# Performance work log

Hardware: AMD Instinct MI355X
Metric: run time of the kernel (lower is better)

The kernel has to match this reference:

```python
import jax, jax.numpy as jnp
import numpy as np


def setup_inputs() -> dict:
    key = jax.random.key(0)
    ks = jax.random.split(key, 6)
    B, C, S, E = 8, 16, 512, 256
    wscale = (2.0 / (E + E)) ** 0.5  # xavier_normal for [E, E] fan_in=fan_out=E
    return {
        "query": jax.random.normal(ks[0], (B, C, S, E), dtype=jnp.float32),
        "key": jax.random.normal(ks[1], (B, C, S, E), dtype=jnp.float32),
        "value": jax.random.normal(ks[2], (B, C, S, E), dtype=jnp.float32),
        "q_proj_weight": jax.random.normal(ks[3], (C, E, E), dtype=jnp.float32) * wscale,
        "k_proj_weight": jax.random.normal(ks[4], (C, E, E), dtype=jnp.float32) * wscale,
        "v_proj_weight": jax.random.normal(ks[5], (C, E, E), dtype=jnp.float32) * wscale,
        "q_proj_bias": jnp.zeros((C, 1, E), dtype=jnp.float32),
        "k_proj_bias": jnp.zeros((C, 1, E), dtype=jnp.float32),
        "v_proj_bias": jnp.zeros((C, 1, E), dtype=jnp.float32),
    }


def reference(query, key, value, q_proj_weight, k_proj_weight, v_proj_weight,
              q_proj_bias, k_proj_bias, v_proj_bias):
    E = query.shape[-1]
    # Per-cycle projection + bias + ReLU.  b=batch, c=cycle, s/t=seq, e/f=embed
    q = jax.nn.relu(jnp.einsum("bcse,cef->bcsf", query, q_proj_weight) + q_proj_bias)
    k = jax.nn.relu(jnp.einsum("bcse,cef->bcsf", key, k_proj_weight) + k_proj_bias)
    v = jax.nn.relu(jnp.einsum("bcse,cef->bcsf", value, v_proj_weight) + v_proj_bias)
    q = q * (float(E) ** -0.5)
    attn = jax.nn.softmax(jnp.einsum("bcse,bcte->bcst", q, k), axis=-1)
    out = jnp.einsum("bcst,bcte->bcse", attn, v)
    return out
```

## Files before the change

kernel.cpp:

```cpp
#include <hip/hip_runtime.h>

constexpr int BATCH = 8;
constexpr int CYC   = 16;
constexpr int SEQ   = 512;
constexpr int EMB   = 256;

typedef __attribute__((ext_vector_type(8))) short bf16x8;
typedef __attribute__((ext_vector_type(4))) float f32x4;

__device__ __forceinline__ unsigned short f2bf(float x) {
    unsigned int u = __float_as_uint(x);
    u += 0x7fffu + ((u >> 16) & 1u);
    return (unsigned short)(u >> 16);
}
__device__ __forceinline__ unsigned int pk2(float lo, float hi) {
    return (unsigned int)f2bf(lo) | ((unsigned int)f2bf(hi) << 16);
}
__device__ __forceinline__ f32x4 mfma16(bf16x8 a, bf16x8 b, f32x4 c) {
    return __builtin_amdgcn_mfma_f32_16x16x32_bf16(a, b, c, 0, 0, 0);
}
__device__ __forceinline__ void gll16(const void* g, void* l) {
    __builtin_amdgcn_global_load_lds(
        (const __attribute__((address_space(1))) void*)g,
        (__attribute__((address_space(3))) void*)l, 16, 0, 0);
}
union BCast { int4 i; bf16x8 v; };

__global__ __launch_bounds__(256) void wt_kernel(
    const float* __restrict__ Wq, const float* __restrict__ Wk,
    const float* __restrict__ Wv,
    unsigned short* __restrict__ Tq, unsigned short* __restrict__ Tk,
    unsigned short* __restrict__ Tv)
{
    __shared__ float tile[64][65];
    const int z = blockIdx.z;
    const int which = z >> 4, c = z & 15;
    const float* W = which == 0 ? Wq : which == 1 ? Wk : Wv;
    unsigned short* Wt = which == 0 ? Tq : which == 1 ? Tk : Tv;
    const int e0 = blockIdx.x * 64;
    const int f0 = blockIdx.y * 64;
    const float* Wc = W + (size_t)c * EMB * EMB;
    unsigned short* Wtc = Wt + (size_t)c * EMB * EMB;
    const int t = threadIdx.x;
    {
        const int er = t >> 4;
        const int fc = (t & 15) * 4;
        for (int i = 0; i < 4; ++i) {
            const float4 v = *(const float4*)(Wc + (size_t)(e0 + er + i * 16) * EMB + f0 + fc);
            tile[er + i * 16][fc + 0] = v.x;
            tile[er + i * 16][fc + 1] = v.y;
            tile[er + i * 16][fc + 2] = v.z;
            tile[er + i * 16][fc + 3] = v.w;
        }
    }
    __syncthreads();
    {
        const int fr = t >> 4;
        const int ec = (t & 15) * 4;
        for (int i = 0; i < 4; ++i) {
            const int f = fr + i * 16;
            ushort4 o;
            o.x = f2bf(tile[ec + 0][f]);
            o.y = f2bf(tile[ec + 1][f]);
            o.z = f2bf(tile[ec + 2][f]);
            o.w = f2bf(tile[ec + 3][f]);
            *(ushort4*)(Wtc + (size_t)(f0 + f) * EMB + e0 + ec) = o;
        }
    }
}

__global__ __launch_bounds__(256, 3) void proj_kernel(
    const float* __restrict__ Xq, const float* __restrict__ Xk,
    const float* __restrict__ Xv,
    const unsigned short* __restrict__ Wq, const unsigned short* __restrict__ Wk,
    const unsigned short* __restrict__ Wv,
    const float* __restrict__ Bq, const float* __restrict__ Bk,
    const float* __restrict__ Bv,
    unsigned short* __restrict__ Yq, unsigned short* __restrict__ Yk,
    unsigned short* __restrict__ Yv)
{
    __shared__ float          As[2][64 * 32];
    __shared__ unsigned short Bs[2][256 * 32];

    const int z = blockIdx.z;
    const float* X = z == 0 ? Xq : z == 1 ? Xk : Xv;
    const unsigned short* Wt = z == 0 ? Wq : z == 1 ? Wk : Wv;
    const float* bias = z == 0 ? Bq : z == 1 ? Bk : Bv;
    unsigned short* Y = z == 0 ? Yq : z == 1 ? Yk : Yv;
    const float scale = z == 0 ? 0.0625f : 1.0f;

    const int bc = blockIdx.x;
    const int c  = bc & (CYC - 1);
    const int m0 = blockIdx.y * 64;
    const float* Xb = X + (size_t)bc * SEQ * EMB;
    const unsigned short* Wc = Wt + (size_t)c * EMB * EMB;
    const float* bb = bias + (size_t)c * EMB;
    unsigned short* Yb = Y + (size_t)bc * SEQ * EMB;

    const int tid  = threadIdx.x;
    const int lane = tid & 63, w = tid >> 6;
    const int ln   = lane & 15, quad = lane >> 4;
    const int wu   = __builtin_amdgcn_readfirstlane(w);

    const int arow = lane >> 3;
    const int achk = (lane & 7) ^ arow;
    const int brow = lane >> 2;
    const int gch  = (lane & 3) ^ ((lane >> 3) & 3);
    const int s8    = ln & 7;
    const int bslot = quad ^ ((ln >> 1) & 3);

    f32x4 acc[4][4];
    for (int i = 0; i < 4; ++i)
        for (int j = 0; j < 4; ++j) acc[i][j] = (f32x4){0.f, 0.f, 0.f, 0.f};

    auto stage = [&](int kk, int b) {
        const int k0 = kk * 32;
#pragma unroll
        for (int j = 0; j < 2; ++j) {
            const int r0 = wu * 16 + j * 8;
            gll16(Xb + (size_t)(m0 + r0 + arow) * EMB + k0 + achk * 4,
                  &As[b][r0 * 32]);
        }
#pragma unroll
        for (int j = 0; j < 4; ++j) {
            const int r0 = wu * 64 + j * 16;
            gll16(Wc + (size_t)(r0 + brow) * EMB + k0 + gch * 8,
                  &Bs[b][r0 * 32]);
        }
    };

    stage(0, 0);
#pragma unroll
    for (int kk = 0; kk < 8; ++kk) {
        const int cur = kk & 1;
        if (kk < 7) {
            stage(kk + 1, cur ^ 1);
            asm volatile("s_waitcnt vmcnt(6)" ::: "memory");
        } else {
            asm volatile("s_waitcnt vmcnt(0)" ::: "memory");
        }
        __builtin_amdgcn_s_barrier();
        __builtin_amdgcn_sched_barrier(0);

        bf16x8 af[4], bfv[4];
#pragma unroll
        for (int i = 0; i < 4; ++i) {
            const float* ar = &As[cur][(i * 16 + ln) * 32];
            const float4 f0 = *(const float4*)(ar + ((2 * quad)     ^ s8) * 4);
            const float4 f1 = *(const float4*)(ar + ((2 * quad + 1) ^ s8) * 4);
            BCast u;
            u.i.x = pk2(f0.x, f0.y); u.i.y = pk2(f0.z, f0.w);
            u.i.z = pk2(f1.x, f1.y); u.i.w = pk2(f1.z, f1.w);
            af[i] = u.v;
        }
#pragma unroll
        for (int j = 0; j < 4; ++j)
            bfv[j] = *(const bf16x8*)&Bs[cur][(w * 64 + j * 16 + ln) * 32 + bslot * 8];
#pragma unroll
        for (int i = 0; i < 4; ++i)
#pragma unroll
            for (int j = 0; j < 4; ++j)
                acc[i][j] = mfma16(af[i], bfv[j], acc[i][j]);

        __builtin_amdgcn_sched_barrier(0);
        asm volatile("s_waitcnt lgkmcnt(0)" ::: "memory");
        __builtin_amdgcn_s_barrier();
    }

    float bvj[4];
#pragma unroll
    for (int j = 0; j < 4; ++j) bvj[j] = bb[w * 64 + j * 16 + ln];

    if (z != 2) {
        unsigned short* ep = (unsigned short*)&As[0][0] + w * 1152;
        for (int i = 0; i < 4; ++i) {
            for (int j = 0; j < 4; ++j)
                for (int r = 0; r < 4; ++r)
                    ep[(quad * 4 + r) * 72 + j * 16 + ln] =
                        f2bf(fmaxf(acc[i][j][r] + bvj[j], 0.f) * scale);
            __syncthreads();
            for (int h = 0; h < 2; ++h) {
                const int cid = lane + h * 64;
                const int row = cid >> 3, ch = cid & 7;
                *(bf16x8*)&Yb[(size_t)(m0 + i * 16 + row) * EMB + w * 64 + ch * 8] =
                    *(const bf16x8*)&ep[row * 72 + ch * 8];
            }
            __syncthreads();
        }
    } else {
        for (int j = 0; j < 4; ++j) {
            const int fg = w * 64 + j * 16 + ln;
            for (int i = 0; i < 4; ++i) {
                const int mb = m0 + i * 16 + quad * 4;
                ushort4 u;
                u.x = f2bf(fmaxf(acc[i][j][0] + bvj[j], 0.f) * scale);
                u.y = f2bf(fmaxf(acc[i][j][1] + bvj[j], 0.f) * scale);
                u.z = f2bf(fmaxf(acc[i][j][2] + bvj[j], 0.f) * scale);
                u.w = f2bf(fmaxf(acc[i][j][3] + bvj[j], 0.f) * scale);
                *(ushort4*)&Yb[(size_t)fg * SEQ + mb] = u;
            }
        }
    }
}

__global__ __launch_bounds__(256) void attn_kernel(
    const unsigned short* __restrict__ Qp, const unsigned short* __restrict__ Kp,
    const unsigned short* __restrict__ Vt, float* __restrict__ Out)
{
    __shared__ unsigned short Ks[32][264];
    __shared__ unsigned short Vs[256][40];
    __shared__ unsigned short Ps[64][40];
    const int bc = blockIdx.x;
    const int qt = blockIdx.y;
    const unsigned short* Qb = Qp + (size_t)bc * SEQ * EMB;
    const unsigned short* Kb = Kp + (size_t)bc * SEQ * EMB;
    const unsigned short* Vb = Vt + (size_t)bc * SEQ * EMB;
    float* Ob = Out + (size_t)bc * SEQ * EMB;

    const int tid  = threadIdx.x;
    const int lane = tid & 63, w = tid >> 6;
    const int ln   = lane & 15, quad = lane >> 4;

    bf16x8 qf[8];
    const int qrow = qt * 64 + w * 16 + ln;
#pragma unroll
    for (int ke = 0; ke < 8; ++ke)
        qf[ke] = *(const bf16x8*)(Qb + (size_t)qrow * EMB + ke * 32 + quad * 8);

    f32x4 of[16];
    for (int n = 0; n < 16; ++n) of[n] = (f32x4){0.f, 0.f, 0.f, 0.f};
    float lsum[4] = {0.f, 0.f, 0.f, 0.f};

    bf16x8 kreg[4], vreg[4];
    auto loadKV = [&](int tt) {
        const int t0 = tt * 32;
#pragma unroll
        for (int i = 0; i < 4; ++i) {
            const int idx = tid + i * 256;
            const int r = idx >> 5, c8 = (idx & 31) * 8;
            kreg[i] = *(const bf16x8*)(Kb + (size_t)(t0 + r) * EMB + c8);
        }
#pragma unroll
        for (int i = 0; i < 4; ++i) {
            const int idx = tid + i * 256;
            const int e = idx >> 2, c8 = (idx & 3) * 8;
            vreg[i] = *(const bf16x8*)(Vb + (size_t)e * SEQ + t0 + c8);
        }
    };
    loadKV(0);

    for (int tt = 0; tt < 16; ++tt) {
#pragma unroll
        for (int i = 0; i < 4; ++i) {
            const int idx = tid + i * 256;
            const int r = idx >> 5, c8 = (idx & 31) * 8;
            *(bf16x8*)&Ks[r][c8] = kreg[i];
        }
#pragma unroll
        for (int i = 0; i < 4; ++i) {
            const int idx = tid + i * 256;
            const int e = idx >> 2, c8 = (idx & 3) * 8;
            *(bf16x8*)&Vs[e][c8] = vreg[i];
        }
        __syncthreads();
        if (tt < 15) loadKV(tt + 1);

        f32x4 sf0 = (f32x4){0.f,0.f,0.f,0.f}, sf1 = (f32x4){0.f,0.f,0.f,0.f};
#pragma unroll
        for (int ke = 0; ke < 8; ++ke) {
            bf16x8 b0 = *(const bf16x8*)&Ks[ln][ke * 32 + quad * 8];
            bf16x8 b1 = *(const bf16x8*)&Ks[16 + ln][ke * 32 + quad * 8];
            sf0 = mfma16(qf[ke], b0, sf0);
            sf1 = mfma16(qf[ke], b1, sf1);
        }

        float p0[4], p1[4];
#pragma unroll
        for (int r = 0; r < 4; ++r) {
            p0[r] = __expf(sf0[r]);
            p1[r] = __expf(sf1[r]);
            lsum[r] += p0[r] + p1[r];
        }
#pragma unroll
        for (int r = 0; r < 4; ++r) {
            Ps[w * 16 + quad * 4 + r][ln]      = f2bf(p0[r]);
            Ps[w * 16 + quad * 4 + r][16 + ln] = f2bf(p1[r]);
        }
        __syncthreads();

        bf16x8 af = *(const bf16x8*)&Ps[w * 16 + ln][quad * 8];
#pragma unroll
        for (int n = 0; n < 16; ++n) {
            bf16x8 bv = *(const bf16x8*)&Vs[n * 16 + ln][quad * 8];
            of[n] = mfma16(af, bv, of[n]);
        }
        __syncthreads();
    }

    for (int off = 1; off < 16; off <<= 1)
        for (int r = 0; r < 4; ++r)
            lsum[r] += __shfl_xor(lsum[r], off, 64);
    float inv[4];
    for (int r = 0; r < 4; ++r) inv[r] = 1.0f / lsum[r];
    const int mbase = qt * 64 + w * 16 + quad * 4;
    for (int n = 0; n < 16; ++n)
        for (int r = 0; r < 4; ++r)
            Ob[(size_t)(mbase + r) * EMB + n * 16 + ln] = of[n][r] * inv[r];
}

extern "C" void kernel_launch(void* const* d_in, const int* in_sizes, int n_in,
                              void* d_out, int out_size, void* d_ws, size_t ws_size,
                              hipStream_t stream) {
    const float* query = (const float*)d_in[0];
    const float* key_  = (const float*)d_in[1];
    const float* value = (const float*)d_in[2];
    const float* wq = (const float*)d_in[3];
    const float* wk = (const float*)d_in[4];
    const float* wv = (const float*)d_in[5];
    const float* bq = (const float*)d_in[6];
    const float* bk = (const float*)d_in[7];
    const float* bv = (const float*)d_in[8];
    float* out = (float*)d_out;

    char* ws = (char*)d_ws;
    const size_t wsz = (size_t)CYC * EMB * EMB * sizeof(unsigned short);
    const size_t psz = (size_t)BATCH * CYC * SEQ * EMB * sizeof(unsigned short);
    unsigned short* Wtq = (unsigned short*)(ws);
    unsigned short* Wtk = (unsigned short*)(ws + wsz);
    unsigned short* Wtv = (unsigned short*)(ws + 2 * wsz);
    unsigned short* Qp  = (unsigned short*)(ws + 3 * wsz);
    unsigned short* Kp  = (unsigned short*)(ws + 3 * wsz + psz);
    unsigned short* Vtp = (unsigned short*)(ws + 3 * wsz + 2 * psz);

    const dim3 tb(256);
    wt_kernel<<<dim3(4, 4, 3 * CYC), tb, 0, stream>>>(wq, wk, wv, Wtq, Wtk, Wtv);

    proj_kernel<<<dim3(BATCH * CYC, SEQ / 64, 3), tb, 0, stream>>>(
        query, key_, value, Wtq, Wtk, Wtv, bq, bk, bv, Qp, Kp, Vtp);

    attn_kernel<<<dim3(BATCH * CYC, SEQ / 64), tb, 0, stream>>>(Qp, Kp, Vtp, out);
}
```

Before: 335.0 us.

## Convert activations to bf16 in registers before LDS, drop attention prefetch, split weight transpose

The projection kernel now loads fp32 activations into registers, packs them to bf16 and stores them to LDS, replacing the async global-to-LDS load of fp32 data. This halves the LDS footprint for A and performs each conversion once per element instead of inside the MFMA fragment reads. Occupancy is raised to 4 blocks per SIMD, and the epilogue scratch moves to the B buffer. The attention kernel drops its register-prefetch double buffering and several unroll pragmas, which risks exposing global load latency. The weight transpose is split into three separate launches.

```diff
diff --git a/kernel.cpp b/kernel.cpp
--- a/kernel.cpp
+++ b/kernel.cpp
@@ -24,19 +24,11 @@
         (const __attribute__((address_space(1))) void*)g,
         (__attribute__((address_space(3))) void*)l, 16, 0, 0);
 }
-union BCast { int4 i; bf16x8 v; };
-
-__global__ __launch_bounds__(256) void wt_kernel(
-    const float* __restrict__ Wq, const float* __restrict__ Wk,
-    const float* __restrict__ Wv,
-    unsigned short* __restrict__ Tq, unsigned short* __restrict__ Tk,
-    unsigned short* __restrict__ Tv)
-{
+
+__global__ __launch_bounds__(256) void wt_kernel(const float* __restrict__ W,
+                                                 unsigned short* __restrict__ Wt) {
     __shared__ float tile[64][65];
-    const int z = blockIdx.z;
-    const int which = z >> 4, c = z & 15;
-    const float* W = which == 0 ? Wq : which == 1 ? Wk : Wv;
-    unsigned short* Wt = which == 0 ? Tq : which == 1 ? Tk : Tv;
+    const int c  = blockIdx.z;
     const int e0 = blockIdx.x * 64;
     const int f0 = blockIdx.y * 64;
     const float* Wc = W + (size_t)c * EMB * EMB;
@@ -69,7 +61,7 @@
     }
 }
 
-__global__ __launch_bounds__(256, 3) void proj_kernel(
+__global__ __launch_bounds__(256, 4) void proj_kernel(
     const float* __restrict__ Xq, const float* __restrict__ Xk,
     const float* __restrict__ Xv,
     const unsigned short* __restrict__ Wq, const unsigned short* __restrict__ Wk,
@@ -79,7 +71,7 @@
     unsigned short* __restrict__ Yq, unsigned short* __restrict__ Yk,
     unsigned short* __restrict__ Yv)
 {
-    __shared__ float          As[2][64 * 32];
+    __shared__ unsigned short As[2][64 * 32];
     __shared__ unsigned short Bs[2][256 * 32];
 
     const int z = blockIdx.z;
@@ -102,25 +94,25 @@
     const int ln   = lane & 15, quad = lane >> 4;
     const int wu   = __builtin_amdgcn_readfirstlane(w);
 
-    const int arow = lane >> 3;
-    const int achk = (lane & 7) ^ arow;
+    const int ar = tid >> 2, ac = (tid & 3) * 8;
     const int brow = lane >> 2;
     const int gch  = (lane & 3) ^ ((lane >> 3) & 3);
-    const int s8    = ln & 7;
     const int bslot = quad ^ ((ln >> 1) & 3);
 
     f32x4 acc[4][4];
     for (int i = 0; i < 4; ++i)
         for (int j = 0; j < 4; ++j) acc[i][j] = (f32x4){0.f, 0.f, 0.f, 0.f};
 
-    auto stage = [&](int kk, int b) {
+    const float* aptr = Xb + (size_t)(m0 + ar) * EMB + ac;
+    float4 a0, a1;
+
+    auto aload = [&](int kk) {
+        const float* p = aptr + kk * 32;
+        a0 = *(const float4*)p;
+        a1 = *(const float4*)(p + 4);
+    };
+    auto bstage = [&](int kk, int b) {
         const int k0 = kk * 32;
-#pragma unroll
-        for (int j = 0; j < 2; ++j) {
-            const int r0 = wu * 16 + j * 8;
-            gll16(Xb + (size_t)(m0 + r0 + arow) * EMB + k0 + achk * 4,
-                  &As[b][r0 * 32]);
-        }
 #pragma unroll
         for (int j = 0; j < 4; ++j) {
             const int r0 = wu * 64 + j * 16;
@@ -129,30 +121,36 @@
         }
     };
 
-    stage(0, 0);
+    aload(0);
+    __builtin_amdgcn_sched_barrier(0);
+    bstage(0, 0);
+
 #pragma unroll
     for (int kk = 0; kk < 8; ++kk) {
         const int cur = kk & 1;
+        asm volatile("s_waitcnt vmcnt(4)" ::: "memory");
+        {
+            int4 pk;
+            pk.x = pk2(a0.x, a0.y); pk.y = pk2(a0.z, a0.w);
+            pk.z = pk2(a1.x, a1.y); pk.w = pk2(a1.z, a1.w);
+            *(int4*)&As[cur][ar * 32 + ac] = pk;
+        }
         if (kk < 7) {
-            stage(kk + 1, cur ^ 1);
+            aload(kk + 1);
+            __builtin_amdgcn_sched_barrier(0);
+            bstage(kk + 1, cur ^ 1);
             asm volatile("s_waitcnt vmcnt(6)" ::: "memory");
         } else {
             asm volatile("s_waitcnt vmcnt(0)" ::: "memory");
         }
+        asm volatile("s_waitcnt lgkmcnt(0)" ::: "memory");
         __builtin_amdgcn_s_barrier();
         __builtin_amdgcn_sched_barrier(0);
 
         bf16x8 af[4], bfv[4];
 #pragma unroll
-        for (int i = 0; i < 4; ++i) {
-            const float* ar = &As[cur][(i * 16 + ln) * 32];
-            const float4 f0 = *(const float4*)(ar + ((2 * quad)     ^ s8) * 4);
-            const float4 f1 = *(const float4*)(ar + ((2 * quad + 1) ^ s8) * 4);
-            BCast u;
-            u.i.x = pk2(f0.x, f0.y); u.i.y = pk2(f0.z, f0.w);
-            u.i.z = pk2(f1.x, f1.y); u.i.w = pk2(f1.z, f1.w);
-            af[i] = u.v;
-        }
+        for (int i = 0; i < 4; ++i)
+            af[i] = *(const bf16x8*)&As[cur][(i * 16 + ln) * 32 + quad * 8];
 #pragma unroll
         for (int j = 0; j < 4; ++j)
             bfv[j] = *(const bf16x8*)&Bs[cur][(w * 64 + j * 16 + ln) * 32 + bslot * 8];
@@ -172,7 +170,7 @@
     for (int j = 0; j < 4; ++j) bvj[j] = bb[w * 64 + j * 16 + ln];
 
     if (z != 2) {
-        unsigned short* ep = (unsigned short*)&As[0][0] + w * 1152;
+        unsigned short* ep = &Bs[0][0] + w * 1152;
         for (int i = 0; i < 4; ++i) {
             for (int j = 0; j < 4; ++j)
                 for (int r = 0; r < 4; ++r)
@@ -223,7 +221,6 @@
 
     bf16x8 qf[8];
     const int qrow = qt * 64 + w * 16 + ln;
-#pragma unroll
     for (int ke = 0; ke < 8; ++ke)
         qf[ke] = *(const bf16x8*)(Qb + (size_t)qrow * EMB + ke * 32 + quad * 8);
 
@@ -231,42 +228,21 @@
     for (int n = 0; n < 16; ++n) of[n] = (f32x4){0.f, 0.f, 0.f, 0.f};
     float lsum[4] = {0.f, 0.f, 0.f, 0.f};
 
-    bf16x8 kreg[4], vreg[4];
-    auto loadKV = [&](int tt) {
+    for (int tt = 0; tt < 16; ++tt) {
         const int t0 = tt * 32;
-#pragma unroll
         for (int i = 0; i < 4; ++i) {
             const int idx = tid + i * 256;
             const int r = idx >> 5, c8 = (idx & 31) * 8;
-            kreg[i] = *(const bf16x8*)(Kb + (size_t)(t0 + r) * EMB + c8);
-        }
-#pragma unroll
+            *(bf16x8*)&Ks[r][c8] = *(const bf16x8*)(Kb + (size_t)(t0 + r) * EMB + c8);
+        }
         for (int i = 0; i < 4; ++i) {
             const int idx = tid + i * 256;
             const int e = idx >> 2, c8 = (idx & 3) * 8;
-            vreg[i] = *(const bf16x8*)(Vb + (size_t)e * SEQ + t0 + c8);
-        }
-    };
-    loadKV(0);
-
-    for (int tt = 0; tt < 16; ++tt) {
-#pragma unroll
-        for (int i = 0; i < 4; ++i) {
-            const int idx = tid + i * 256;
-            const int r = idx >> 5, c8 = (idx & 31) * 8;
-            *(bf16x8*)&Ks[r][c8] = kreg[i];
-        }
-#pragma unroll
-        for (int i = 0; i < 4; ++i) {
-            const int idx = tid + i * 256;
-            const int e = idx >> 2, c8 = (idx & 3) * 8;
-            *(bf16x8*)&Vs[e][c8] = vreg[i];
+            *(bf16x8*)&Vs[e][c8] = *(const bf16x8*)(Vb + (size_t)e * SEQ + t0 + c8);
         }
         __syncthreads();
-        if (tt < 15) loadKV(tt + 1);
 
         f32x4 sf0 = (f32x4){0.f,0.f,0.f,0.f}, sf1 = (f32x4){0.f,0.f,0.f,0.f};
-#pragma unroll
         for (int ke = 0; ke < 8; ++ke) {
             bf16x8 b0 = *(const bf16x8*)&Ks[ln][ke * 32 + quad * 8];
             bf16x8 b1 = *(const bf16x8*)&Ks[16 + ln][ke * 32 + quad * 8];
@@ -275,13 +251,11 @@
         }
 
         float p0[4], p1[4];
-#pragma unroll
         for (int r = 0; r < 4; ++r) {
             p0[r] = __expf(sf0[r]);
             p1[r] = __expf(sf1[r]);
             lsum[r] += p0[r] + p1[r];
         }
-#pragma unroll
         for (int r = 0; r < 4; ++r) {
             Ps[w * 16 + quad * 4 + r][ln]      = f2bf(p0[r]);
             Ps[w * 16 + quad * 4 + r][16 + ln] = f2bf(p1[r]);
@@ -289,7 +263,6 @@
         __syncthreads();
 
         bf16x8 af = *(const bf16x8*)&Ps[w * 16 + ln][quad * 8];
-#pragma unroll
         for (int n = 0; n < 16; ++n) {
             bf16x8 bv = *(const bf16x8*)&Vs[n * 16 + ln][quad * 8];
             of[n] = mfma16(af, bv, of[n]);
@@ -333,7 +306,9 @@
     unsigned short* Vtp = (unsigned short*)(ws + 3 * wsz + 2 * psz);
 
     const dim3 tb(256);
-    wt_kernel<<<dim3(4, 4, 3 * CYC), tb, 0, stream>>>(wq, wk, wv, Wtq, Wtk, Wtv);
+    wt_kernel<<<dim3(4, 4, CYC), tb, 0, stream>>>(wq, Wtq);
+    wt_kernel<<<dim3(4, 4, CYC), tb, 0, stream>>>(wk, Wtk);
+    wt_kernel<<<dim3(4, 4, CYC), tb, 0, stream>>>(wv, Wtv);
 
     proj_kernel<<<dim3(BATCH * CYC, SEQ / 64, 3), tb, 0, stream>>>(
         query, key_, value, Wtq, Wtk, Wtv, bq, bk, bv, Qp, Kp, Vtp);
```

New measurement: 338.2 us. No clear change (+1.0%).
